# Kernel tuning notes

Hardware: AMD Instinct MI355X
Metric: run time of the kernel (lower is better)

## Reference

```python
import jax, jax.numpy as jnp
import numpy as np

N_NODES = 100000
N_EDGES = 3200000
N_FEAT = 128
N_HID = 64


def gcn_conv(x, src, dst, ew, W, b, n):
    # x: [N, Fin]; src/dst: [E'] incl. self-loops; ew: [E'] edge weights
    xw = x @ W  # [N, Fout]
    deg = jax.ops.segment_sum(ew, dst, num_segments=n)  # [N]
    dinv = jnp.where(deg > 0, jax.lax.rsqrt(jnp.maximum(deg, 1e-12)), 0.0)
    norm = dinv[src] * ew * dinv[dst]  # [E']
    out = jax.ops.segment_sum(norm[:, None] * xw[src], dst, num_segments=n)
    return out + b


def setup_inputs() -> dict:
    key = jax.random.key(0)
    k = jax.random.split(key, 8)
    x = jax.random.normal(k[0], (N_NODES, N_FEAT), dtype=jnp.float32)
    edge_index = jax.random.randint(k[1], (2, N_EDGES), 0, N_NODES, dtype=jnp.int32)
    edge_attr = jax.random.uniform(k[2], (N_EDGES,), dtype=jnp.float32)
    s1 = 1.0 / np.sqrt(N_FEAT)
    s2 = 1.0 / np.sqrt(N_HID)
    W1 = jax.random.uniform(k[3], (N_FEAT, N_HID), minval=-s1, maxval=s1, dtype=jnp.float32)
    b1 = jnp.zeros((N_HID,), dtype=jnp.float32)
    W2 = jax.random.uniform(k[4], (N_HID, 1), minval=-s2, maxval=s2, dtype=jnp.float32)
    b2 = jnp.zeros((1,), dtype=jnp.float32)
    return {"x": x, "edge_index": edge_index, "edge_attr": edge_attr,
            "W1": W1, "b1": b1, "W2": W2, "b2": b2}


def reference(x, edge_index, edge_attr, W1, b1, W2, b2):
    n = x.shape[0]
    # add self-loops with weight 1 (PyG gcn_norm, improved=False)
    loop = jnp.arange(n, dtype=edge_index.dtype)
    src = jnp.concatenate([edge_index[0], loop])
    dst = jnp.concatenate([edge_index[1], loop])
    ew = jnp.concatenate([edge_attr, jnp.ones((n,), dtype=edge_attr.dtype)])
    h = gcn_conv(x, src, dst, ew, W1, b1, n)
    h = jax.nn.relu(h)
    # dropout is identity in eval mode
    out = gcn_conv(h, src, dst, ew, W2, b2, n)
    return out
```

## Files before the change

kernel.cpp:

```cpp
#include <hip/hip_runtime.h>
#include <hip/hip_fp16.h>


#define NPB_LOG 9
#define NPB     512
#define PCAP    17408
#define NEDG    8192
#define GPAD    16

typedef _Float16 f16x8 __attribute__((ext_vector_type(8)));
typedef float    f32x4 __attribute__((ext_vector_type(4)));

__global__ void k_initcur(int* __restrict__ gcur, int npart) {
    int i = blockIdx.x * blockDim.x + threadIdx.x;
    if (i < npart) gcur[i * GPAD] = i * PCAP;
}

__global__ __launch_bounds__(256) void k_binA(const int* __restrict__ src,
                                              const int* __restrict__ dst,
                                              const float* __restrict__ ea,
                                              int* __restrict__ gcur,
                                              uint2* __restrict__ part,
                                              int E, int npart) {
    __shared__ uint2 stag[NEDG];
    __shared__ unsigned char stagb[NEDG];
    __shared__ int hist[256];
    __shared__ int lofs[256];
    __shared__ int base[256];
    int t = threadIdx.x;
    int c0 = blockIdx.x * NEDG;
    hist[t] = 0;
    __syncthreads();
    for (int j = t; j < NEDG; j += 256) {
        int e = c0 + j;
        if (e < E) atomicAdd(&hist[dst[e] >> NPB_LOG], 1);
    }
    __syncthreads();
    int v = hist[t];
    lofs[t] = v;
    __syncthreads();
    for (int off = 1; off < 256; off <<= 1) {
        int u = (t >= off) ? lofs[t - off] : 0;
        __syncthreads();
        lofs[t] += u;
        __syncthreads();
    }
    int excl = lofs[t] - v;
    if (t < npart && v > 0) base[t] = atomicAdd(&gcur[t * GPAD], v);
    __syncthreads();
    lofs[t] = excl;
    hist[t] = excl;
    __syncthreads();
    for (int j = t; j < NEDG; j += 256) {
        int e = c0 + j;
        if (e < E) {
            int d = dst[e];
            int b = d >> NPB_LOG;
            int p = atomicAdd(&hist[b], 1);
            stag[p]  = make_uint2((uint)src[e] | ((uint)(d & (NPB - 1)) << 17),
                                  __float_as_uint(ea[e]));
            stagb[p] = (unsigned char)b;
        }
    }
    __syncthreads();
    int nvalid = min(NEDG, E - c0);
    for (int j = t; j < nvalid; j += 256) {
        int b = stagb[j];
        int gp = base[b] + (j - lofs[b]);
        if (gp < (b + 1) * PCAP) part[gp] = stag[j];
    }
}

__global__ __launch_bounds__(512) void k_binB(const int* __restrict__ gcur,
                                              const uint2* __restrict__ part,
                                              int2* __restrict__ ecsr,
                                              int2* __restrict__ rowdesc,
                                              float* __restrict__ dinv, int n) {
    __shared__ uint2 stag[PCAP];
    __shared__ int   cnt[NPB];
    __shared__ float wsum[NPB];
    __shared__ int   cur[NPB];
    __shared__ int   wsums[8];
    int b = blockIdx.x;
    int t = threadIdx.x;
    int lane = t & 63, wv = t >> 6;
    cnt[t] = 0; wsum[t] = 0.0f;
    __syncthreads();
    int beg = b * PCAP;
    int len = gcur[b * GPAD] - beg;
    if (len > PCAP) len = PCAP;
    for (int j = t; j < len; j += NPB) {
        uint2 ed = part[beg + j];
        stag[j] = ed;
        int dlow = (ed.x >> 17) & (NPB - 1);
        atomicAdd(&cnt[dlow], 1);
        atomicAdd(&wsum[dlow], __uint_as_float(ed.y));
    }
    __syncthreads();
    int v = cnt[t];
    int s = v;
    for (int off = 1; off < 64; off <<= 1) {
        int u = __shfl_up(s, off, 64);
        if (lane >= off) s += u;
    }
    if (lane == 63) wsums[wv] = s;
    __syncthreads();
    if (t < 64) {
        int x = (t < 8) ? wsums[t] : 0;
        for (int off = 1; off < 8; off <<= 1) {
            int u = __shfl_up(x, off, 64);
            if (lane >= off) x += u;
        }
        if (t < 8) wsums[t] = x;
    }
    __syncthreads();
    int excl = s - v + (wv > 0 ? wsums[wv - 1] : 0);
    cur[t] = excl;
    int node = (b << NPB_LOG) + t;
    if (node < n) {
        rowdesc[node] = make_int2(beg + excl, v);
        dinv[node]    = rsqrtf(1.0f + wsum[t]);
    }
    __syncthreads();
    for (int j = t; j < len; j += NPB) {
        uint2 ed = stag[j];
        int dlow = (ed.x >> 17) & (NPB - 1);
        int p = atomicAdd(&cur[dlow], 1);
        ecsr[beg + p] = make_int2((int)(ed.x & 0x1FFFF), (int)ed.y);
    }
}

#define XPAD 136
__global__ __launch_bounds__(256) void k_gemm1m(const float* __restrict__ x,
                                                const float* __restrict__ W1,
                                                const float* __restrict__ dinv,
                                                __half* __restrict__ xw2, int n) {
    __shared__ __align__(16) _Float16 xs[64 * XPAD];
    __shared__ __align__(16) _Float16 wt[64 * XPAD];
    int tid = threadIdx.x;
    int row0 = blockIdx.x * 64;
    for (int i = tid; i < 64 * 32; i += 256) {
        int r = i >> 5, k4 = i & 31;
        float4 f = make_float4(0.f, 0.f, 0.f, 0.f);
        int gr = row0 + r;
        if (gr < n) f = ((const float4*)x)[(size_t)gr * 32 + k4];
        union { _Float16 h[4]; uint2 u; } tmp;
        tmp.h[0] = (_Float16)f.x; tmp.h[1] = (_Float16)f.y;
        tmp.h[2] = (_Float16)f.z; tmp.h[3] = (_Float16)f.w;
        *(uint2*)&xs[r * XPAD + k4 * 4] = tmp.u;
    }
    for (int i = tid; i < 128 * 64; i += 256) {
        int k = i >> 6, nn = i & 63;
        wt[nn * XPAD + k] = (_Float16)W1[i];
    }
    __syncthreads();

    int strip = tid >> 6;
    int lane  = tid & 63;
    int quad  = lane >> 4;
    int m     = lane & 15;
    f32x4 acc[4] = {{0,0,0,0},{0,0,0,0},{0,0,0,0},{0,0,0,0}};
#pragma unroll
    for (int kc = 0; kc < 4; ++kc) {
        f16x8 a = *(const f16x8*)&xs[(strip * 16 + m) * XPAD + kc * 32 + quad * 8];
#pragma unroll
        for (int nt = 0; nt < 4; ++nt) {
            f16x8 b = *(const f16x8*)&wt[(nt * 16 + m) * XPAD + kc * 32 + quad * 8];
            acc[nt] = __builtin_amdgcn_mfma_f32_16x16x32_f16(a, b, acc[nt], 0, 0, 0);
        }
    }
    float dv[4];
#pragma unroll
    for (int reg = 0; reg < 4; ++reg) {
        int gr = row0 + strip * 16 + quad * 4 + reg;
        dv[reg] = (gr < n) ? dinv[gr] : 0.0f;
    }
#pragma unroll
    for (int nt = 0; nt < 4; ++nt) {
#pragma unroll
        for (int reg = 0; reg < 4; ++reg) {
            int gr = row0 + strip * 16 + quad * 4 + reg;
            if (gr < n)
                xw2[(size_t)gr * 64 + nt * 16 + m] = __float2half(dv[reg] * acc[nt][reg]);
        }
    }
}

__global__ __launch_bounds__(256) void k_agg1f(const int2* __restrict__ rowdesc,
                                               const int2* __restrict__ ecsr,
                                               const float* __restrict__ dinv,
                                               const __half* __restrict__ xw2,
                                               const float* __restrict__ b1,
                                               const float* __restrict__ W2,
                                               float* __restrict__ g, int n) {
    int i = blockIdx.x * 4 + (threadIdx.x >> 6);
    int lane = threadIdx.x & 63;
    if (i >= n) return;
    int2 rd = rowdesc[i];
    int beg = __builtin_amdgcn_readfirstlane(rd.x);
    int len = __builtin_amdgcn_readfirstlane(rd.y);
    const int2* __restrict__ ep = ecsr + beg;

    float a0 = __half2float(xw2[(size_t)i * 64 + lane]);
    float a1 = 0.0f, a2 = 0.0f, a3 = 0.0f;
    int j = 0;
    for (; j + 8 <= len; j += 8) {
        int2 e0 = ep[j + 0];
        int2 e1 = ep[j + 1];
        int2 e2 = ep[j + 2];
        int2 e3 = ep[j + 3];
        int2 e4 = ep[j + 4];
        int2 e5 = ep[j + 5];
        int2 e6 = ep[j + 6];
        int2 e7 = ep[j + 7];
        float v0 = __half2float(xw2[(size_t)(uint)e0.x * 64 + lane]);
        float v1 = __half2float(xw2[(size_t)(uint)e1.x * 64 + lane]);
        float v2 = __half2float(xw2[(size_t)(uint)e2.x * 64 + lane]);
        float v3 = __half2float(xw2[(size_t)(uint)e3.x * 64 + lane]);
        float v4 = __half2float(xw2[(size_t)(uint)e4.x * 64 + lane]);
        float v5 = __half2float(xw2[(size_t)(uint)e5.x * 64 + lane]);
        float v6 = __half2float(xw2[(size_t)(uint)e6.x * 64 + lane]);
        float v7 = __half2float(xw2[(size_t)(uint)e7.x * 64 + lane]);
        a0 += __int_as_float(e0.y) * v0;
        a1 += __int_as_float(e1.y) * v1;
        a2 += __int_as_float(e2.y) * v2;
        a3 += __int_as_float(e3.y) * v3;
        a0 += __int_as_float(e4.y) * v4;
        a1 += __int_as_float(e5.y) * v5;
        a2 += __int_as_float(e6.y) * v6;
        a3 += __int_as_float(e7.y) * v7;
    }
    for (; j < len; ++j) {
        int2 e = ep[j];
        a0 += __int_as_float(e.y) * __half2float(xw2[(size_t)(uint)e.x * 64 + lane]);
    }
    float acc = (a0 + a1) + (a2 + a3);
    float di = dinv[i];
    float h = fmaxf(di * acc + b1[lane], 0.0f) * W2[lane];
    for (int off = 32; off; off >>= 1) h += __shfl_down(h, off, 64);
    if (lane == 0) g[i] = di * h;
}

__global__ __launch_bounds__(256) void k_agg2(const int2* __restrict__ rowdesc,
                                              const int2* __restrict__ ecsr,
                                              const float* __restrict__ dinv,
                                              const float* __restrict__ g,
                                              const float* __restrict__ b2,
                                              float* __restrict__ out, int n) {
    int i = blockIdx.x * 4 + (threadIdx.x >> 6);
    int lane = threadIdx.x & 63;
    if (i >= n) return;
    int2 rd = rowdesc[i];
    int beg = __builtin_amdgcn_readfirstlane(rd.x);
    int len = __builtin_amdgcn_readfirstlane(rd.y);
    const int2* __restrict__ ep = ecsr + beg;
    float p = 0.0f;
    for (int j = lane; j < len; j += 64) {
        int2 ed = ep[j];
        p += __int_as_float(ed.y) * g[ed.x];
    }
    for (int off = 32; off; off >>= 1) p += __shfl_down(p, off, 64);
    if (lane == 0) out[i] = b2[0] + dinv[i] * (g[i] + p);
}

extern "C" void kernel_launch(void* const* d_in, const int* in_sizes, int n_in,
                              void* d_out, int out_size, void* d_ws, size_t ws_size,
                              hipStream_t stream) {
    const float* x  = (const float*)d_in[0];
    const int*   ei = (const int*)  d_in[1];
    const float* ea = (const float*)d_in[2];
    const float* W1 = (const float*)d_in[3];
    const float* b1 = (const float*)d_in[4];
    const float* W2 = (const float*)d_in[5];
    const float* b2 = (const float*)d_in[6];
    float* out = (float*)d_out;

    int n = in_sizes[0] / 128;
    int E = in_sizes[1] / 2;
    const int* src = ei;
    const int* dst = ei + E;
    int npart = (n + NPB - 1) >> NPB_LOG;

    int*    ws       = (int*)d_ws;
    int*    gcur     = ws;
    uint2*  part     = (uint2*)(ws + 256 * GPAD);
    __half* xw2      = (__half*)part;
    size_t  psz      = (size_t)npart * PCAP;
    int2*   ecsr     = (int2*)(ws + 256 * GPAD + psz * 2);
    int2*   rowdesc  = (int2*)(ws + 256 * GPAD + psz * 4);
    float*  dinv     = (float*)(ws + 256 * GPAD + psz * 4 + (size_t)2 * n);
    float*  g        = dinv + n;

    k_initcur<<<1, 256, 0, stream>>>(gcur, npart);
    k_binA  <<<(E + NEDG - 1) / NEDG, 256, 0, stream>>>(src, dst, ea, gcur, part, E, npart);
    k_binB  <<<npart, NPB, 0, stream>>>(gcur, part, ecsr, rowdesc, dinv, n);
    k_gemm1m<<<(n + 63) / 64, 256, 0, stream>>>(x, W1, dinv, xw2, n);
    k_agg1f <<<(n + 3) / 4, 256, 0, stream>>>(rowdesc, ecsr, dinv, xw2, b1, W2, g, n);
    k_agg2  <<<(n + 3) / 4, 256, 0, stream>>>(rowdesc, ecsr, dinv, g, b2, out, n);
}
```

Measured before the change: 317.1 us.

## Merge GEMM into binning kernel and apply dinv scaling in binB

The XW1 GEMM blocks now run inside the binning kernel launch as extra blocks, so they can overlap the edge-partitioning work instead of running as a separate launch after binB. Because dinv is not known until binB, the GEMM writes unscaled fp16 results, and binB rescales each of its nodes' rows in place by dinv after building the CSR. The CSR is written in place over the partition buffer, which frees workspace for a separate xw2 region. The cost is a larger shared-memory footprint per block (76.8KB for all blocks) and an extra fp16 read-modify-write pass with a second rounding.

Result: no change. 319.5 us (+0.8%).

```diff
diff --git a/kernel.cpp b/kernel.cpp
--- a/kernel.cpp
+++ b/kernel.cpp
@@ -7,6 +7,7 @@
 #define PCAP    17408
 #define NEDG    8192
 #define GPAD    16
+#define XPAD    136
 
 typedef _Float16 f16x8 __attribute__((ext_vector_type(8)));
 typedef float    f32x4 __attribute__((ext_vector_type(4)));
@@ -16,18 +17,66 @@
     if (i < npart) gcur[i * GPAD] = i * PCAP;
 }
 
-__global__ __launch_bounds__(256) void k_binA(const int* __restrict__ src,
-                                              const int* __restrict__ dst,
-                                              const float* __restrict__ ea,
-                                              int* __restrict__ gcur,
-                                              uint2* __restrict__ part,
-                                              int E, int npart) {
-    __shared__ uint2 stag[NEDG];
-    __shared__ unsigned char stagb[NEDG];
-    __shared__ int hist[256];
-    __shared__ int lofs[256];
-    __shared__ int base[256];
+__global__ __launch_bounds__(256) void k_binA_gemm(
+        const int* __restrict__ src, const int* __restrict__ dst,
+        const float* __restrict__ ea, int* __restrict__ gcur,
+        uint2* __restrict__ part,
+        const float* __restrict__ x, const float* __restrict__ W1,
+        __half* __restrict__ xw2,
+        int E, int npart, int nA, int n) {
+    __shared__ __align__(16) unsigned char smem[76800];
     int t = threadIdx.x;
+
+    if (blockIdx.x >= nA) {
+        _Float16* xs = (_Float16*)smem;
+        _Float16* wt = xs + 64 * XPAD;
+        int row0 = (blockIdx.x - nA) * 64;
+        for (int i = t; i < 64 * 32; i += 256) {
+            int r = i >> 5, k4 = i & 31;
+            float4 f = make_float4(0.f, 0.f, 0.f, 0.f);
+            int gr = row0 + r;
+            if (gr < n) f = ((const float4*)x)[(size_t)gr * 32 + k4];
+            union { _Float16 h[4]; uint2 u; } tmp;
+            tmp.h[0] = (_Float16)f.x; tmp.h[1] = (_Float16)f.y;
+            tmp.h[2] = (_Float16)f.z; tmp.h[3] = (_Float16)f.w;
+            *(uint2*)&xs[r * XPAD + k4 * 4] = tmp.u;
+        }
+        for (int i = t; i < 128 * 64; i += 256) {
+            int k = i >> 6, nn = i & 63;
+            wt[nn * XPAD + k] = (_Float16)W1[i];
+        }
+        __syncthreads();
+        int strip = t >> 6;
+        int lane  = t & 63;
+        int quad  = lane >> 4;
+        int m     = lane & 15;
+        f32x4 acc[4] = {{0,0,0,0},{0,0,0,0},{0,0,0,0},{0,0,0,0}};
+#pragma unroll
+        for (int kc = 0; kc < 4; ++kc) {
+            f16x8 a = *(const f16x8*)&xs[(strip * 16 + m) * XPAD + kc * 32 + quad * 8];
+#pragma unroll
+            for (int nt = 0; nt < 4; ++nt) {
+                f16x8 b = *(const f16x8*)&wt[(nt * 16 + m) * XPAD + kc * 32 + quad * 8];
+                acc[nt] = __builtin_amdgcn_mfma_f32_16x16x32_f16(a, b, acc[nt], 0, 0, 0);
+            }
+        }
+#pragma unroll
+        for (int nt = 0; nt < 4; ++nt) {
+#pragma unroll
+            for (int reg = 0; reg < 4; ++reg) {
+                int gr = row0 + strip * 16 + quad * 4 + reg;
+                if (gr < n)
+                    xw2[(size_t)gr * 64 + nt * 16 + m] = __float2half(acc[nt][reg]);
+            }
+        }
+        return;
+    }
+
+    uint2*         stag  = (uint2*)smem;
+    unsigned char* stagb = smem + 65536;
+    int*           hist  = (int*)(smem + 73728);
+    int*           lofs  = hist + 256;
+    int*           base  = lofs + 256;
     int c0 = blockIdx.x * NEDG;
     hist[t] = 0;
     __syncthreads();
@@ -72,10 +121,10 @@
 }
 
 __global__ __launch_bounds__(512) void k_binB(const int* __restrict__ gcur,
-                                              const uint2* __restrict__ part,
-                                              int2* __restrict__ ecsr,
+                                              uint2* __restrict__ part,
                                               int2* __restrict__ rowdesc,
-                                              float* __restrict__ dinv, int n) {
+                                              float* __restrict__ dinv,
+                                              __half* __restrict__ xw2, int n) {
     __shared__ uint2 stag[PCAP];
     __shared__ int   cnt[NPB];
     __shared__ float wsum[NPB];
@@ -116,72 +165,36 @@
     __syncthreads();
     int excl = s - v + (wv > 0 ? wsums[wv - 1] : 0);
     cur[t] = excl;
+    float dval = rsqrtf(1.0f + wsum[t]);
     int node = (b << NPB_LOG) + t;
     if (node < n) {
         rowdesc[node] = make_int2(beg + excl, v);
-        dinv[node]    = rsqrtf(1.0f + wsum[t]);
-    }
+        dinv[node]    = dval;
+    }
+    wsum[t] = dval;
     __syncthreads();
     for (int j = t; j < len; j += NPB) {
         uint2 ed = stag[j];
         int dlow = (ed.x >> 17) & (NPB - 1);
         int p = atomicAdd(&cur[dlow], 1);
-        ecsr[beg + p] = make_int2((int)(ed.x & 0x1FFFF), (int)ed.y);
-    }
-}
-
-#define XPAD 136
-__global__ __launch_bounds__(256) void k_gemm1m(const float* __restrict__ x,
-                                                const float* __restrict__ W1,
-                                                const float* __restrict__ dinv,
-                                                __half* __restrict__ xw2, int n) {
-    __shared__ __align__(16) _Float16 xs[64 * XPAD];
-    __shared__ __align__(16) _Float16 wt[64 * XPAD];
-    int tid = threadIdx.x;
-    int row0 = blockIdx.x * 64;
-    for (int i = tid; i < 64 * 32; i += 256) {
-        int r = i >> 5, k4 = i & 31;
-        float4 f = make_float4(0.f, 0.f, 0.f, 0.f);
-        int gr = row0 + r;
-        if (gr < n) f = ((const float4*)x)[(size_t)gr * 32 + k4];
-        union { _Float16 h[4]; uint2 u; } tmp;
-        tmp.h[0] = (_Float16)f.x; tmp.h[1] = (_Float16)f.y;
-        tmp.h[2] = (_Float16)f.z; tmp.h[3] = (_Float16)f.w;
-        *(uint2*)&xs[r * XPAD + k4 * 4] = tmp.u;
-    }
-    for (int i = tid; i < 128 * 64; i += 256) {
-        int k = i >> 6, nn = i & 63;
-        wt[nn * XPAD + k] = (_Float16)W1[i];
-    }
-    __syncthreads();
-
-    int strip = tid >> 6;
-    int lane  = tid & 63;
-    int quad  = lane >> 4;
-    int m     = lane & 15;
-    f32x4 acc[4] = {{0,0,0,0},{0,0,0,0},{0,0,0,0},{0,0,0,0}};
-#pragma unroll
-    for (int kc = 0; kc < 4; ++kc) {
-        f16x8 a = *(const f16x8*)&xs[(strip * 16 + m) * XPAD + kc * 32 + quad * 8];
-#pragma unroll
-        for (int nt = 0; nt < 4; ++nt) {
-            f16x8 b = *(const f16x8*)&wt[(nt * 16 + m) * XPAD + kc * 32 + quad * 8];
-            acc[nt] = __builtin_amdgcn_mfma_f32_16x16x32_f16(a, b, acc[nt], 0, 0, 0);
-        }
-    }
-    float dv[4];
-#pragma unroll
-    for (int reg = 0; reg < 4; ++reg) {
-        int gr = row0 + strip * 16 + quad * 4 + reg;
-        dv[reg] = (gr < n) ? dinv[gr] : 0.0f;
-    }
-#pragma unroll
-    for (int nt = 0; nt < 4; ++nt) {
-#pragma unroll
-        for (int reg = 0; reg < 4; ++reg) {
-            int gr = row0 + strip * 16 + quad * 4 + reg;
-            if (gr < n)
-                xw2[(size_t)gr * 64 + nt * 16 + m] = __float2half(dv[reg] * acc[nt][reg]);
+        ((int2*)part)[beg + p] = make_int2((int)(ed.x & 0x1FFFF), (int)ed.y);
+    }
+    int node0 = b << NPB_LOG;
+    int nrows = n - node0;
+    if (nrows > NPB) nrows = NPB;
+    if (nrows > 0) {
+        uint2* xp = (uint2*)(xw2 + (size_t)node0 * 64);
+        int tot = nrows * 16;
+        for (int j = t; j < tot; j += NPB) {
+            float d = wsum[j >> 4];
+            uint2 u = xp[j];
+            __half2* h = (__half2*)&u;
+#pragma unroll
+            for (int k = 0; k < 2; ++k) {
+                float2 f = __half22float2(h[k]);
+                h[k] = __floats2half2_rn(f.x * d, f.y * d);
+            }
+            xp[j] = u;
         }
     }
 }
@@ -280,21 +293,23 @@
     const int* src = ei;
     const int* dst = ei + E;
     int npart = (n + NPB - 1) >> NPB_LOG;
+    int nA = (E + NEDG - 1) / NEDG;
+    int nG = (n + 63) / 64;
 
     int*    ws       = (int*)d_ws;
     int*    gcur     = ws;
     uint2*  part     = (uint2*)(ws + 256 * GPAD);
-    __half* xw2      = (__half*)part;
     size_t  psz      = (size_t)npart * PCAP;
-    int2*   ecsr     = (int2*)(ws + 256 * GPAD + psz * 2);
-    int2*   rowdesc  = (int2*)(ws + 256 * GPAD + psz * 4);
-    float*  dinv     = (float*)(ws + 256 * GPAD + psz * 4 + (size_t)2 * n);
+    __half* xw2      = (__half*)(ws + 256 * GPAD + psz * 2);
+    int2*   rowdesc  = (int2*)(ws + 256 * GPAD + psz * 2 + (size_t)32 * n);
+    float*  dinv     = (float*)(ws + 256 * GPAD + psz * 2 + (size_t)34 * n);
     float*  g        = dinv + n;
-
-    k_initcur<<<1, 256, 0, stream>>>(gcur, npart);
-    k_binA  <<<(E + NEDG - 1) / NEDG, 256, 0, stream>>>(src, dst, ea, gcur, part, E, npart);
-    k_binB  <<<npart, NPB, 0, stream>>>(gcur, part, ecsr, rowdesc, dinv, n);
-    k_gemm1m<<<(n + 63) / 64, 256, 0, stream>>>(x, W1, dinv, xw2, n);
-    k_agg1f <<<(n + 3) / 4, 256, 0, stream>>>(rowdesc, ecsr, dinv, xw2, b1, W2, g, n);
-    k_agg2  <<<(n + 3) / 4, 256, 0, stream>>>(rowdesc, ecsr, dinv, g, b2, out, n);
-}
+    int2*   ecsr     = (int2*)part;
+
+    k_initcur  <<<1, 256, 0, stream>>>(gcur, npart);
+    k_binA_gemm<<<nA + nG, 256, 0, stream>>>(src, dst, ea, gcur, part,
+                                             x, W1, xw2, E, npart, nA, n);
+    k_binB     <<<npart, NPB, 0, stream>>>(gcur, part, rowdesc, dinv, xw2, n);
+    k_agg1f    <<<(n + 3) / 4, 256, 0, stream>>>(rowdesc, ecsr, dinv, xw2, b1, W2, g, n);
+    k_agg2     <<<(n + 3) / 4, 256, 0, stream>>>(rowdesc, ecsr, dinv, g, b2, out, n);
+}
```
